# Kernel optimization log

Measured on AMD Instinct MI355X. Metric: run time of the kernel, lower is better.

The kernel has to match this reference:

```python
import jax, jax.numpy as jnp
import numpy as np

B, N_PER, E_PER = 100, 1000, 12000  # graphs, nodes/graph, edges/graph
N, E = B * N_PER, B * E_PER
K = int(np.ceil(0.8 * N_PER))  # TopKPooling ratio=0.8 -> 800 kept nodes/graph


def setup_inputs() -> dict:
    key = jax.random.key(0)
    ks = jax.random.split(key, 16)
    g = jnp.repeat(jnp.arange(B, dtype=jnp.int64), E_PER)
    src = g * N_PER + jax.random.randint(ks[0], (E,), 0, N_PER)
    dst = g * N_PER + jax.random.randint(ks[1], (E,), 0, N_PER)
    edge_index = jnp.stack([src, dst]).astype(jnp.int64)
    edge_attr = jax.random.uniform(ks[2], (E,), dtype=jnp.float32) + 0.1  # positive edge weights
    x = jax.random.normal(ks[3], (N, 3), dtype=jnp.float32)
    batch = jnp.repeat(jnp.arange(B, dtype=jnp.int64), N_PER)
    s = 0.1
    return {
        'x': x, 'edge_index': edge_index, 'edge_attr': edge_attr, 'batch': batch,
        'conv1_w': jax.random.normal(ks[4], (3, 64), dtype=jnp.float32) * s,
        'conv1_b': jnp.zeros((64,), dtype=jnp.float32),
        'conv2_w': jax.random.normal(ks[5], (64, 64), dtype=jnp.float32) * s,
        'conv2_b': jnp.zeros((64,), dtype=jnp.float32),
        'pool_w': jax.random.normal(ks[6], (64,), dtype=jnp.float32) * s,
        'lin1_w': jax.random.normal(ks[7], (64, 64), dtype=jnp.float32) * s,
        'lin1_b': jnp.zeros((64,), dtype=jnp.float32),
        'lin2_w': jax.random.normal(ks[8], (64, 32), dtype=jnp.float32) * s,
        'lin2_b': jnp.zeros((32,), dtype=jnp.float32),
        'lin3_w': jax.random.normal(ks[9], (32, 1), dtype=jnp.float32) * s,
        'lin3_b': jnp.zeros((1,), dtype=jnp.float32),
    }


def gcn_conv(x, row, col, ew, W, b):
    # PyG GCNConv with edge_weight and implicit self-loops (weight 1):
    # deg[i] = sum_{e: col=i} ew[e] + 1;  norm_e = d^{-1/2}[row]*ew*d^{-1/2}[col]
    h = x @ W  # [N, out]
    deg = jax.ops.segment_sum(ew, col, num_segments=N) + 1.0
    dinv = jax.lax.rsqrt(deg)
    msg = (dinv[row] * ew * dinv[col])[:, None] * h[row]  # [E, out]
    out = jax.ops.segment_sum(msg, col, num_segments=N)
    out = out + (dinv * dinv)[:, None] * h  # self-loop term
    return out + b


def reference(x, edge_index, edge_attr, batch, conv1_w, conv1_b, conv2_w, conv2_b,
              pool_w, lin1_w, lin1_b, lin2_w, lin2_b, lin3_w, lin3_b):
    row, col = edge_index[0], edge_index[1]
    h = jax.nn.relu(gcn_conv(x, row, col, edge_attr, conv1_w, conv1_b))
    x1 = h.reshape(B, N_PER, 64).mean(axis=1)  # global_mean_pool (equal-size graphs)
    h = jax.nn.relu(gcn_conv(h, row, col, edge_attr, conv2_w, conv2_b))
    # TopKPooling: score = tanh(x.w / ||w||), keep top-K per graph, gate by score
    score = jnp.tanh(h @ pool_w / jnp.linalg.norm(pool_w))  # [N]
    score_bn = score.reshape(B, N_PER)
    vals, idx = jax.lax.top_k(score_bn, K)  # [B, K]
    h_bn = h.reshape(B, N_PER, 64)
    h_sel = jnp.take_along_axis(h_bn, idx[..., None], axis=1) * vals[..., None]
    x2 = h_sel.mean(axis=1)  # global_mean_pool on pooled graph
    z = x1 + x2
    z = jax.nn.relu(z @ lin1_w + lin1_b)
    z = jax.nn.relu(z @ lin2_w + lin2_b)  # dropout is identity in eval mode
    out = jax.nn.sigmoid(z @ lin3_w + lin3_b)[:, 0]
    return out
```

## Files before the change

kernel.cpp:

```cpp
#include <hip/hip_runtime.h>

#define B_G   100
#define N_PER 1000
#define E_PER 12000
#define NTOT  (B_G * N_PER)
#define ETOT  (B_G * E_PER)
#define KSEL  800
#define EPT   12

typedef __attribute__((ext_vector_type(8))) short short8;
typedef __attribute__((ext_vector_type(4))) float float4_;

__device__ __forceinline__ unsigned short f2bf(float f) {
    unsigned u = __float_as_uint(f);
    u += 0x7fffu + ((u >> 16) & 1u);
    return (unsigned short)(u >> 16);
}
__device__ __forceinline__ float upk(unsigned q) {
    return __uint_as_float(q & 0xFFFF0000u);
}
__device__ __forceinline__ float dec_raw(unsigned byte7f) {
    return __uint_as_float(byte7f << 20);
}
__device__ __forceinline__ unsigned enc_fp8(float z) {
    unsigned u = __float_as_uint(z * 0x1p-120f);
    u += 0x7FFFFu + ((u >> 20) & 1u);
    return u >> 20;
}

__global__ __launch_bounds__(1024) void k_all(
    const int* __restrict__ ei, const float* __restrict__ ew,
    const float* __restrict__ x,
    const float* __restrict__ w1, const float* __restrict__ b1,
    const float* __restrict__ w2, const float* __restrict__ b2,
    const float* __restrict__ pw,
    const float* __restrict__ l1w, const float* __restrict__ l1b,
    const float* __restrict__ l2w, const float* __restrict__ l2b,
    const float* __restrict__ l3w, const float* __restrict__ l3b,
    float* __restrict__ out) {
    __shared__ __align__(16) unsigned char smem[136832];
    unsigned char* zs = smem;
    float* xl = (float*)smem;
    unsigned* csr = (unsigned*)(smem + 64000);
    int*   ends = (int*)(smem + 112000);
    float* dl   = (float*)(smem + 116096);
    int*   posc = (int*)(smem + 116096);
    int*   wpart = (int*)(smem + 120192);
    float* x1b   = (float*)(smem + 120192);
    unsigned char* uA = smem + 120448;
    float* aggv = (float*)uA;

    int b = blockIdx.x, tid = threadIdx.x;
    int wid = tid >> 6, lane = tid & 63;
    int gbase = b * N_PER, ebase = b * E_PER;

    int esrc[EPT], edst[EPT]; float eww[EPT];
    int ne = (tid < (E_PER - (EPT - 1) * 1024)) ? EPT : EPT - 1;
#pragma unroll
    for (int i = 0; i < EPT; i++) {
        if (i < ne) {
            int e = tid + i * 1024;
            esrc[i] = ei[ebase + e] - gbase;
            edst[i] = ei[ETOT + ebase + e] - gbase;
            eww[i]  = ew[ebase + e];
        }
    }
    ends[tid] = 0;
    for (int i = tid; i < N_PER * 3; i += 1024) xl[i] = x[(size_t)gbase * 3 + i];
    __syncthreads();
#pragma unroll
    for (int i = 0; i < EPT; i++)
        if (i < ne) atomicAdd(&ends[edst[i]], 1);
    __syncthreads();
    int v = ends[tid];
    int sc = v;
#pragma unroll
    for (int m = 1; m < 64; m <<= 1) {
        int t = __shfl_up(sc, m);
        if (lane >= m) sc += t;
    }
    if (lane == 63) wpart[wid] = sc;
    __syncthreads();
    if (tid < 16) {
        int s2 = wpart[tid];
#pragma unroll
        for (int m = 1; m < 16; m <<= 1) {
            int t = __shfl_up(s2, m);
            if (tid >= m) s2 += t;
        }
        wpart[tid] = s2;
    }
    __syncthreads();
    int incl = sc + (wid > 0 ? wpart[wid - 1] : 0);
    ends[tid] = incl;
    posc[tid] = incl - v;
    __syncthreads();
#pragma unroll
    for (int i = 0; i < EPT; i++)
        if (i < ne) {
            int p = atomicAdd(&posc[edst[i]], 1);
            csr[p] = ((unsigned)f2bf(eww[i]) << 16) | (unsigned)esrc[i];
        }
    __syncthreads();
    float dmy = 0.f;
    int s0i = 0, e0i = 0;
    if (tid < N_PER) {
        s0i = tid ? ends[tid - 1] : 0;
        e0i = ends[tid];
        float s0 = 0.f, s1 = 0.f;
        int k = s0i;
        for (; k + 2 <= e0i; k += 2) { s0 += upk(csr[k]); s1 += upk(csr[k + 1]); }
        if (k < e0i) s0 += upk(csr[k]);
        dmy = rsqrtf(s0 + s1 + 1.0f);
        dl[tid] = dmy;
        xl[tid * 3 + 0] *= dmy;
        xl[tid * 3 + 1] *= dmy;
        xl[tid * 3 + 2] *= dmy;
    }
    __syncthreads();
    if (tid < N_PER) {
        float a0 = xl[tid * 3 + 0], a1 = xl[tid * 3 + 1], a2 = xl[tid * 3 + 2];
        for (int k = s0i; k < e0i; k++) {
            unsigned q = csr[k];
            int i0 = (int)(q & 0xFFFFu) * 3;
            float wv = upk(q);
            a0 += wv * xl[i0]; a1 += wv * xl[i0 + 1]; a2 += wv * xl[i0 + 2];
        }
        aggv[tid * 3 + 0] = dmy * a0;
        aggv[tid * 3 + 1] = dmy * a1;
        aggv[tid * 3 + 2] = dmy * a2;
    }
    __syncthreads();
    {
        float w0 = w1[lane], w1v = w1[64 + lane], w2v = w1[128 + lane], bf = b1[lane];
        float* sred = (float*)(uA + 12288);
        float px = 0.f;
        int chunk = (lane & 31) >> 3;
        int word  = ((lane >= 32) ? 2 : 0) + ((lane & 7) >> 2);
        for (int node = wid; node < N_PER; node += 16) {
            float a0 = aggv[node * 3], a1 = aggv[node * 3 + 1], a2 = aggv[node * 3 + 2];
            float hv = fmaxf(a0 * w0 + a1 * w1v + a2 * w2v + bf, 0.f);
            px += hv;
            unsigned byte = enc_fp8(dl[node] * hv);
            unsigned t1 = __shfl_xor(byte, 1);
            unsigned v16 = (lane & 1) ? (t1 | (byte << 8)) : (byte | (t1 << 8));
            unsigned t2 = __shfl_xor(v16, 2);
            unsigned v32 = (lane & 2) ? (t2 | (v16 << 16)) : (v16 | (t2 << 16));
            if ((lane & 3) == 0) {
                int cs = chunk ^ ((node >> 1) & 3);
                *(unsigned*)(zs + node * 64 + cs * 16 + word * 4) = v32;
            }
        }
        sred[wid * 64 + lane] = px;
        __syncthreads();
        if (tid < 64) {
            float t = 0.f;
            for (int r = 0; r < 16; r++) t += sred[r * 64 + tid];
            x1b[tid] = t * (1.0f / N_PER);
        }
    }
    int kgrp = lane >> 4, nloc = lane & 15;
    short8 AfS[4][2];
#pragma unroll
    for (int ti = 0; ti < 4; ti++) {
        int t = wid + ti * 16;
        int li = t * 16 + nloc;
        bool valid = li < N_PER;
        float acc[16];
        int s = 0, cn = 0;
        if (valid) {
            uint4 rv = *(const uint4*)(zs + li * 64 + ((kgrp ^ ((li >> 1) & 3)) << 4));
#pragma unroll
            for (int j = 0; j < 4; j++) {
                acc[j]      = dec_raw((rv.x >> (8 * j)) & 0x7Fu);
                acc[4 + j]  = dec_raw((rv.y >> (8 * j)) & 0x7Fu);
                acc[8 + j]  = dec_raw((rv.z >> (8 * j)) & 0x7Fu);
                acc[12 + j] = dec_raw((rv.w >> (8 * j)) & 0x7Fu);
            }
            s = li ? ends[li - 1] : 0;
            cn = ends[li] - s;
        } else {
#pragma unroll
            for (int j = 0; j < 16; j++) acc[j] = 0.f;
        }
        int mx = cn;
#pragma unroll
        for (int m = 1; m < 16; m <<= 1) mx = max(mx, __shfl_xor(mx, m));
        for (int k = 0; k < mx; k++) {
            if (k < cn) {
                unsigned q = csr[s + k];
                int src = (int)(q & 0xFFFFu);
                float wv = upk(q);
                uint4 rv = *(const uint4*)(zs + src * 64 + ((kgrp ^ ((src >> 1) & 3)) << 4));
#pragma unroll
                for (int j = 0; j < 4; j++) {
                    acc[j]      += wv * dec_raw((rv.x >> (8 * j)) & 0x7Fu);
                    acc[4 + j]  += wv * dec_raw((rv.y >> (8 * j)) & 0x7Fu);
                    acc[8 + j]  += wv * dec_raw((rv.z >> (8 * j)) & 0x7Fu);
                    acc[12 + j] += wv * dec_raw((rv.w >> (8 * j)) & 0x7Fu);
                }
            }
        }
        float scale = (valid ? dl[li] : 0.f) * 0x1p120f;
        short8 a0, a1;
#pragma unroll
        for (int j = 0; j < 8; j++) {
            a0[j] = (short)f2bf(scale * acc[j]);
            a1[j] = (short)f2bf(scale * acc[8 + j]);
        }
        AfS[ti][0] = a0;
        AfS[ti][1] = a1;
    }
    __syncthreads();
    unsigned long long* keys = (unsigned long long*)uA;
    {
        short8 Bf[2][4];
#pragma unroll
        for (int kh = 0; kh < 2; ++kh)
#pragma unroll
            for (int c = 0; c < 4; ++c) {
                short8 t;
#pragma unroll
                for (int j = 0; j < 8; ++j)
                    t[j] = (short)f2bf(w2[(kh * 32 + kgrp * 8 + j) * 64 + c * 16 + nloc]);
                Bf[kh][c] = t;
            }
        float b2c[4], pwc[4];
#pragma unroll
        for (int c = 0; c < 4; ++c) {
            b2c[c] = b2[c * 16 + nloc];
            pwc[c] = pw[c * 16 + nloc];
        }
        float invn;
        {
            float p = pw[lane], pn = p * p;
#pragma unroll
            for (int m = 32; m; m >>= 1) pn += __shfl_xor(pn, m);
            invn = rsqrtf(pn);
        }
        if (tid >= N_PER) keys[tid] = 0ull;
#pragma unroll
        for (int ti = 0; ti < 4; ti++) {
            int t = wid + ti * 16;
            if (t >= 63) continue;
            float4_ accv[4];
#pragma unroll
            for (int c = 0; c < 4; ++c) accv[c] = (float4_){0.f, 0.f, 0.f, 0.f};
#pragma unroll
            for (int kh = 0; kh < 2; ++kh)
#pragma unroll
                for (int c = 0; c < 4; ++c)
                    accv[c] = __builtin_amdgcn_mfma_f32_16x16x32_bf16(AfS[ti][kh], Bf[kh][c], accv[c], 0, 0, 0);
#pragma unroll
            for (int r2 = 0; r2 < 4; ++r2) {
                int li2 = t * 16 + kgrp * 4 + r2;
                bool valid2 = li2 < N_PER;
                float sp = 0.f;
#pragma unroll
                for (int c = 0; c < 4; ++c) {
                    float hv = fmaxf(accv[c][r2] + b2c[c], 0.f);
                    sp += hv * pwc[c];
                    if (valid2) zs[li2 * 64 + c * 16 + nloc] = (unsigned char)enc_fp8(hv);
                }
#pragma unroll
                for (int m = 1; m < 16; m <<= 1) sp += __shfl_xor(sp, m);
                if (valid2 && nloc == 0) {
                    float scv = tanhf(sp * invn);
                    unsigned bits = __float_as_uint(scv);
                    unsigned u = (bits & 0x80000000u) ? ~bits : (bits | 0x80000000u);
                    keys[li2] = ((unsigned long long)u << 32) | (unsigned)(1023 - li2);
                }
            }
        }
    }
    __syncthreads();
    {
        unsigned long long key = keys[tid];
        for (int k = 2; k <= 1024; k <<= 1) {
            for (int j = k >> 1; j > 0; j >>= 1) {
                bool desc = (tid & k) == 0;
                unsigned long long p;
                if (j >= 64) {
                    keys[tid] = key;
                    __syncthreads();
                    p = keys[tid ^ j];
                    __syncthreads();
                } else {
                    p = __shfl_xor(key, j);
                }
                bool low = (tid & j) == 0;
                bool sw = low ? (desc ? (key < p) : (key > p))
                              : (desc ? (p < key) : (p > key));
                if (sw) key = p;
            }
        }
        keys[tid] = key;
    }
    __syncthreads();
    float* red   = (float*)(uA + 8192);
    float* a1buf = (float*)(uA + 12288);
    float* a2buf = (float*)(uA + 12544);
    float* zbuf  = (float*)(uA + 12672);
    {
        int f = tid & 63, w16 = tid >> 6;
        float acc2 = 0.f;
        for (int r = w16; r < KSEL; r += 16) {
            unsigned long long key = keys[r];
            int idx = 1023 - (int)(key & 0xFFFFFFFFu);
            unsigned u = (unsigned)(key >> 32);
            unsigned bits = (u & 0x80000000u) ? (u & 0x7FFFFFFFu) : ~u;
            float valS = __uint_as_float(bits) * 0x1p120f;
            acc2 += valS * dec_raw((unsigned)zs[idx * 64 + f] & 0x7Fu);
        }
        red[tid] = acc2;
    }
    __syncthreads();
    if (tid < 64) {
        float s2 = 0.f;
        for (int ww = 0; ww < 16; ww++) s2 += red[ww * 64 + tid];
        zbuf[tid] = x1b[tid] + s2 * (1.0f / KSEL);
    }
    __syncthreads();
    if (tid < 64) {
        float a = l1b[tid];
        for (int k = 0; k < 64; k++) a += zbuf[k] * l1w[k * 64 + tid];
        a1buf[tid] = fmaxf(a, 0.f);
    }
    __syncthreads();
    if (tid < 32) {
        float a = l2b[tid];
        for (int k = 0; k < 64; k++) a += a1buf[k] * l2w[k * 32 + tid];
        a2buf[tid] = fmaxf(a, 0.f);
    }
    __syncthreads();
    if (tid == 0) {
        float t = l3b[0];
        for (int k = 0; k < 32; k++) t += a2buf[k] * l3w[k];
        out[b] = 1.0f / (1.0f + expf(-t));
    }
}

extern "C" void kernel_launch(void* const* d_in, const int* in_sizes, int n_in,
                              void* d_out, int out_size, void* d_ws, size_t ws_size,
                              hipStream_t stream) {
    const float* x   = (const float*)d_in[0];
    const int*   ei  = (const int*)d_in[1];
    const float* ew  = (const float*)d_in[2];
    const float* c1w = (const float*)d_in[4];
    const float* c1b = (const float*)d_in[5];
    const float* c2w = (const float*)d_in[6];
    const float* c2b = (const float*)d_in[7];
    const float* pw  = (const float*)d_in[8];
    const float* l1w = (const float*)d_in[9];
    const float* l1b = (const float*)d_in[10];
    const float* l2w = (const float*)d_in[11];
    const float* l2b = (const float*)d_in[12];
    const float* l3w = (const float*)d_in[13];
    const float* l3b = (const float*)d_in[14];
    float* out = (float*)d_out;
    (void)d_ws; (void)ws_size; (void)in_sizes; (void)n_in; (void)out_size;

    k_all<<<B_G, 1024, 0, stream>>>(ei, ew, x, c1w, c1b, c2w, c2b, pw,
                                    l1w, l1b, l2w, l2b, l3w, l3b, out);
}
```

Before: 181.0 us.

## Fuse conv2 MFMA into aggregation loop, spill h2 to global workspace

Conv2 aggregation and its MFMA transform now run inside the same per-tile loop, so the A fragments are no longer held for all tiles and the block-wide barrier between the two phases is gone. Conv2 weights are staged once in LDS as transposed bf16 instead of being loaded into registers per thread. Because the in-place LDS write of h2 would race with neighbours still being gathered, the fp8 h2 rows are written packed to a global workspace and read back for top-k pooling. This trades register pressure and a sync for extra global traffic and 8 KB more shared memory.

```diff
diff --git a/kernel.cpp b/kernel.cpp
--- a/kernel.cpp
+++ b/kernel.cpp
@@ -37,8 +37,8 @@
     const float* __restrict__ l1w, const float* __restrict__ l1b,
     const float* __restrict__ l2w, const float* __restrict__ l2b,
     const float* __restrict__ l3w, const float* __restrict__ l3b,
-    float* __restrict__ out) {
-    __shared__ __align__(16) unsigned char smem[136832];
+    unsigned char* __restrict__ h2g, float* __restrict__ out) {
+    __shared__ __align__(16) unsigned char smem[145024];
     unsigned char* zs = smem;
     float* xl = (float*)smem;
     unsigned* csr = (unsigned*)(smem + 64000);
@@ -49,6 +49,7 @@
     float* x1b   = (float*)(smem + 120192);
     unsigned char* uA = smem + 120448;
     float* aggv = (float*)uA;
+    unsigned short* w2s = (unsigned short*)(smem + 136832);
 
     int b = blockIdx.x, tid = threadIdx.x;
     int wid = tid >> 6, lane = tid & 63;
@@ -67,6 +68,11 @@
     }
     ends[tid] = 0;
     for (int i = tid; i < N_PER * 3; i += 1024) xl[i] = x[(size_t)gbase * 3 + i];
+    {
+        int n = tid >> 4;
+        for (int k = (tid & 15) * 4, ke = k + 4; k < ke; k++)
+            w2s[n * 64 + k] = f2bf(w2[k * 64 + n]);
+    }
     __syncthreads();
 #pragma unroll
     for (int i = 0; i < EPT; i++)
@@ -160,10 +166,25 @@
         }
     }
     int kgrp = lane >> 4, nloc = lane & 15;
-    short8 AfS[4][2];
-#pragma unroll
+    unsigned long long* keys = (unsigned long long*)uA;
+    if (tid >= N_PER) keys[tid] = 0ull;
+    float b2c[4], pwc[4];
+#pragma unroll
+    for (int c = 0; c < 4; ++c) {
+        b2c[c] = b2[c * 16 + nloc];
+        pwc[c] = pw[c * 16 + nloc];
+    }
+    float invn;
+    {
+        float p = pw[lane], pn = p * p;
+#pragma unroll
+        for (int m = 32; m; m >>= 1) pn += __shfl_xor(pn, m);
+        invn = rsqrtf(pn);
+    }
+#pragma unroll 1
     for (int ti = 0; ti < 4; ti++) {
         int t = wid + ti * 16;
+        if (t >= 63) continue;
         int li = t * 16 + nloc;
         bool valid = li < N_PER;
         float acc[16];
@@ -202,74 +223,40 @@
             }
         }
         float scale = (valid ? dl[li] : 0.f) * 0x1p120f;
-        short8 a0, a1;
+        short8 Af0, Af1;
 #pragma unroll
         for (int j = 0; j < 8; j++) {
-            a0[j] = (short)f2bf(scale * acc[j]);
-            a1[j] = (short)f2bf(scale * acc[8 + j]);
-        }
-        AfS[ti][0] = a0;
-        AfS[ti][1] = a1;
-    }
-    __syncthreads();
-    unsigned long long* keys = (unsigned long long*)uA;
-    {
-        short8 Bf[2][4];
-#pragma unroll
-        for (int kh = 0; kh < 2; ++kh)
+            Af0[j] = (short)f2bf(scale * acc[j]);
+            Af1[j] = (short)f2bf(scale * acc[8 + j]);
+        }
+        float4_ accv[4];
+#pragma unroll
+        for (int c = 0; c < 4; ++c) {
+            const short8* bp = (const short8*)(w2s + (c * 16 + nloc) * 64 + kgrp * 8);
+            accv[c] = __builtin_amdgcn_mfma_f32_16x16x32_bf16(Af0, bp[0], (float4_){0.f,0.f,0.f,0.f}, 0, 0, 0);
+            accv[c] = __builtin_amdgcn_mfma_f32_16x16x32_bf16(Af1, bp[4], accv[c], 0, 0, 0);
+        }
+#pragma unroll
+        for (int r2 = 0; r2 < 4; ++r2) {
+            int li2 = t * 16 + kgrp * 4 + r2;
+            bool valid2 = li2 < N_PER;
+            float sp = 0.f;
+            unsigned pack = 0;
 #pragma unroll
             for (int c = 0; c < 4; ++c) {
-                short8 t;
-#pragma unroll
-                for (int j = 0; j < 8; ++j)
-                    t[j] = (short)f2bf(w2[(kh * 32 + kgrp * 8 + j) * 64 + c * 16 + nloc]);
-                Bf[kh][c] = t;
-            }
-        float b2c[4], pwc[4];
-#pragma unroll
-        for (int c = 0; c < 4; ++c) {
-            b2c[c] = b2[c * 16 + nloc];
-            pwc[c] = pw[c * 16 + nloc];
-        }
-        float invn;
-        {
-            float p = pw[lane], pn = p * p;
-#pragma unroll
-            for (int m = 32; m; m >>= 1) pn += __shfl_xor(pn, m);
-            invn = rsqrtf(pn);
-        }
-        if (tid >= N_PER) keys[tid] = 0ull;
-#pragma unroll
-        for (int ti = 0; ti < 4; ti++) {
-            int t = wid + ti * 16;
-            if (t >= 63) continue;
-            float4_ accv[4];
-#pragma unroll
-            for (int c = 0; c < 4; ++c) accv[c] = (float4_){0.f, 0.f, 0.f, 0.f};
-#pragma unroll
-            for (int kh = 0; kh < 2; ++kh)
-#pragma unroll
-                for (int c = 0; c < 4; ++c)
-                    accv[c] = __builtin_amdgcn_mfma_f32_16x16x32_bf16(AfS[ti][kh], Bf[kh][c], accv[c], 0, 0, 0);
-#pragma unroll
-            for (int r2 = 0; r2 < 4; ++r2) {
-                int li2 = t * 16 + kgrp * 4 + r2;
-                bool valid2 = li2 < N_PER;
-                float sp = 0.f;
-#pragma unroll
-                for (int c = 0; c < 4; ++c) {
-                    float hv = fmaxf(accv[c][r2] + b2c[c], 0.f);
-                    sp += hv * pwc[c];
-                    if (valid2) zs[li2 * 64 + c * 16 + nloc] = (unsigned char)enc_fp8(hv);
-                }
-#pragma unroll
-                for (int m = 1; m < 16; m <<= 1) sp += __shfl_xor(sp, m);
-                if (valid2 && nloc == 0) {
-                    float scv = tanhf(sp * invn);
-                    unsigned bits = __float_as_uint(scv);
-                    unsigned u = (bits & 0x80000000u) ? ~bits : (bits | 0x80000000u);
-                    keys[li2] = ((unsigned long long)u << 32) | (unsigned)(1023 - li2);
-                }
+                float hv = fmaxf(accv[c][r2] + b2c[c], 0.f);
+                sp += hv * pwc[c];
+                pack |= enc_fp8(hv) << (8 * c);
+            }
+            if (valid2)
+                *(unsigned*)(h2g + (size_t)(gbase + li2) * 64 + nloc * 4) = pack;
+#pragma unroll
+            for (int m = 1; m < 16; m <<= 1) sp += __shfl_xor(sp, m);
+            if (valid2 && nloc == 0) {
+                float scv = tanhf(sp * invn);
+                unsigned bits = __float_as_uint(scv);
+                unsigned u = (bits & 0x80000000u) ? ~bits : (bits | 0x80000000u);
+                keys[li2] = ((unsigned long long)u << 32) | (unsigned)(1023 - li2);
             }
         }
     }
@@ -303,6 +290,7 @@
     float* zbuf  = (float*)(uA + 12672);
     {
         int f = tid & 63, w16 = tid >> 6;
+        int boff = ((f & 15) << 2) + (f >> 4);
         float acc2 = 0.f;
         for (int r = w16; r < KSEL; r += 16) {
             unsigned long long key = keys[r];
@@ -310,7 +298,7 @@
             unsigned u = (unsigned)(key >> 32);
             unsigned bits = (u & 0x80000000u) ? (u & 0x7FFFFFFFu) : ~u;
             float valS = __uint_as_float(bits) * 0x1p120f;
-            acc2 += valS * dec_raw((unsigned)zs[idx * 64 + f] & 0x7Fu);
+            acc2 += valS * dec_raw((unsigned)h2g[(size_t)(gbase + idx) * 64 + boff] & 0x7Fu);
         }
         red[tid] = acc2;
     }
@@ -358,8 +346,9 @@
     const float* l3w = (const float*)d_in[13];
     const float* l3b = (const float*)d_in[14];
     float* out = (float*)d_out;
-    (void)d_ws; (void)ws_size; (void)in_sizes; (void)n_in; (void)out_size;
+    unsigned char* h2g = (unsigned char*)d_ws;
+    (void)ws_size; (void)in_sizes; (void)n_in; (void)out_size;
 
     k_all<<<B_G, 1024, 0, stream>>>(ei, ew, x, c1w, c1b, c2w, c2b, pw,
-                                    l1w, l1b, l2w, l2b, l3w, l3b, out);
-}
+                                    l1w, l1b, l2w, l2b, l3w, l3b, h2g, out);
+}
```

Result: slower. 192.6 us (+6.4%).
